# Kernel tuning notes

Measured on AMD Instinct MI355X. Metric: run time of the kernel, lower is better.

The kernel has to match this reference:

```python
import jax, jax.numpy as jnp
import numpy as np

B, T, V, D = 8, 256, 32, 256


def setup_inputs() -> dict:
    key = jax.random.key(0)
    k1, k2 = jax.random.split(key)
    # scale by 0.1 so exp(q.k) stays well within fp32 range (dot std ~ 0.1^2*sqrt(D))
    feature = jax.random.normal(k1, (B, T, V, D), dtype=jnp.float32) * 0.1
    feature_aug = jax.random.normal(k2, (B, T, V, D), dtype=jnp.float32) * 0.1
    return {"feature": feature, "feature_aug": feature_aug}


def reference(feature, feature_aug):
    # match torch permute(0,2,1,3): [B,T,V,D] -> [B,V,T,D]
    f = jnp.transpose(feature, (0, 2, 1, 3))      # [B,V,Tq,D]
    fa = jnp.transpose(feature_aug, (0, 2, 1, 3))  # [B,V,Tk,D]
    # all-pairs QK^T scores: [B_i, B_j, V, Tq, Tk]
    scores = jnp.einsum('ivqd,jvkd->ijvqk', f, fa)
    E = jnp.exp(scores)
    # positive (j == i): ap = exp(scores[i,i]).sum over V, Tq -> [B, Tk]
    diag = jnp.einsum('iivqk->ivqk', E)           # [B,V,Tq,Tk]
    ap_exp = diag.sum(axis=(1, 2))                # [B, Tk]
    # negatives (j != i): sum over j,V,Tk minus the j==i part -> [B, Tq]
    total = E.sum(axis=(1, 2, 4))                 # [B, Tq]
    self_part = diag.sum(axis=(1, 3))             # [B, Tq]
    an_exp = total - self_part                    # [B, Tq]
    # per-anchor loss vector [T]; original sums over anchors then takes .mean()
    loss_vec = -jnp.log(ap_exp / an_exp)          # [B, T]
    return loss_vec.sum(axis=0).mean()
```

## Files before the change

### kernel.cpp

```cpp
#include <hip/hip_runtime.h>
#include <hip/hip_bf16.h>


typedef __attribute__((ext_vector_type(4))) float f32x4;
typedef __attribute__((ext_vector_type(4))) int   i32x4;
typedef __attribute__((ext_vector_type(8))) int   i32x8;
typedef __attribute__((ext_vector_type(8))) __bf16 bf16x8;

#if __has_builtin(__builtin_amdgcn_exp2f)
#define EXP2(x) __builtin_amdgcn_exp2f(x)
#else
#define EXP2(x) exp2f(x)
#endif

__device__ __forceinline__ unsigned short f2bf(float f) {
    unsigned u = __builtin_bit_cast(unsigned, f);
    u += 0x7FFFu + ((u >> 16) & 1u);
    return (unsigned short)(u >> 16);
}

template <bool HI>
__device__ __forceinline__ unsigned cvt2fp8(float a, float b, unsigned old) {
    return __builtin_amdgcn_cvt_pk_fp8_f32(a, b, old, HI);
}
__device__ __forceinline__ unsigned pack4fp8(float x, float y, float z, float w) {
    return cvt2fp8<true>(z, w, cvt2fp8<false>(x, y, 0u));
}

__device__ __forceinline__ void async16(const void* g, void* l) {
    __builtin_amdgcn_global_load_lds(
        (const __attribute__((address_space(1))) unsigned int*)g,
        (__attribute__((address_space(3))) unsigned int*)l,
        16, 0, 0);
}

__device__ __forceinline__ i32x8 cat8(i32x4 lo, i32x4 hi) {
    i32x8 r;
    r[0] = lo[0]; r[1] = lo[1]; r[2] = lo[2]; r[3] = lo[3];
    r[4] = hi[0]; r[5] = hi[1]; r[6] = hi[2]; r[7] = hi[3];
    return r;
}

template <int CTRL>
__device__ __forceinline__ float dpp_add(float x) {
    int y = __builtin_amdgcn_update_dpp(0, __builtin_bit_cast(int, x),
                                        CTRL, 0xf, 0xf, true);
    return x + __builtin_bit_cast(float, y);
}
__device__ __forceinline__ float rowsum16(float x) {
    x = dpp_add<0x111>(x);
    x = dpp_add<0x112>(x);
    x = dpp_add<0x114>(x);
    x = dpp_add<0x118>(x);
    return x;
}

__global__ __launch_bounds__(256) void infonce_repack_fp8(
    const float* __restrict__ feat, const float* __restrict__ feat_aug,
    unsigned char* __restrict__ pA, unsigned char* __restrict__ pB,
    float* __restrict__ counters)
{
    const int row = blockIdx.x;
    const int tid = threadIdx.x;
    if (blockIdx.x == 0 && blockIdx.y == 0) {
        #pragma unroll
        for (int k = 0; k < 24; ++k) counters[k * 256 + tid] = 0.f;
    }
    const bool isA = (blockIdx.y == 0);
    const float sc = isA ? 1.4426950408889634f : 1.0f;
    const float* src = (isA ? feat : feat_aug) + (size_t)row * 8192;
    unsigned char* dst = (isA ? pA : pB) + (size_t)row * 8192;
    #pragma unroll
    for (int it = 0; it < 2; ++it) {
        const int base = it * 4096 + tid * 16;
        const float4 f0 = *(const float4*)(src + base);
        const float4 f1 = *(const float4*)(src + base + 4);
        const float4 f2 = *(const float4*)(src + base + 8);
        const float4 f3 = *(const float4*)(src + base + 12);
        uint4 p;
        p.x = pack4fp8(f0.x*sc, f0.y*sc, f0.z*sc, f0.w*sc);
        p.y = pack4fp8(f1.x*sc, f1.y*sc, f1.z*sc, f1.w*sc);
        p.z = pack4fp8(f2.x*sc, f2.y*sc, f2.z*sc, f2.w*sc);
        p.w = pack4fp8(f3.x*sc, f3.y*sc, f3.z*sc, f3.w*sc);
        *(uint4*)(dst + base) = p;
    }
}

__global__ __launch_bounds__(256, 2) void infonce_main_mx(
    const unsigned char* __restrict__ pA, const unsigned char* __restrict__ pB,
    float* __restrict__ total, float* __restrict__ selfp, float* __restrict__ ap)
{
    __shared__ __align__(16) unsigned char As[128 * 256];
    __shared__ __align__(16) unsigned char Bs[128 * 256];
    float (*ls_row2)[128] = (float (*)[128])(void*)As;
    float (*ls_col2)[128] = (float (*)[128])(void*)(As + 1024);

    const int tid  = threadIdx.x;
    const int lane = tid & 63;
    const int w    = tid >> 6;
    const int wm   = w >> 1;
    const int wn   = w & 1;
    const int lrow = lane & 15;
    const int quad = lane >> 4;

    const int tileM = blockIdx.x & 15;
    const int tileN = blockIdx.x >> 4;
    const int v     = blockIdx.y;
    const bool diag = (tileM >> 1) == (tileN >> 1);

    const size_t vOff = (size_t)v * 256;
    const size_t rowM = (size_t)(tileM * 128 + w * 32 + quad) * 8192 + vOff;
    const size_t rowN = (size_t)(tileN * 128 + w * 32 + quad) * 8192 + vOff;
    #pragma unroll
    for (int i = 0; i < 8; ++i) {
        const int lg = (lrow ^ ((i * 4 + quad) & 15)) << 4;
        async16(pA + rowM + (size_t)i * 4 * 8192 + lg, &As[(w * 32 + i * 4) * 256]);
        async16(pB + rowN + (size_t)i * 4 * 8192 + lg, &Bs[(w * 32 + i * 4) * 256]);
    }

    f32x4 acc[4][4];
    #pragma unroll
    for (int i = 0; i < 4; ++i)
        #pragma unroll
        for (int j = 0; j < 4; ++j)
            acc[i][j] = (f32x4){0.f, 0.f, 0.f, 0.f};

    __syncthreads();

    #pragma unroll
    for (int h = 0; h < 2; ++h) {
        const int g0 = ((h * 8 + quad * 2) ^ lrow) * 16;
        const int g1 = g0 ^ 16;
        i32x8 af[4], bf[4];
        #pragma unroll
        for (int t = 0; t < 4; ++t) {
            const int rA = (wm * 64 + t * 16 + lrow) * 256;
            const int rB = (wn * 64 + t * 16 + lrow) * 256;
            af[t] = cat8(*(const i32x4*)&As[rA + g0], *(const i32x4*)&As[rA + g1]);
            bf[t] = cat8(*(const i32x4*)&Bs[rB + g0], *(const i32x4*)&Bs[rB + g1]);
        }
        #pragma unroll
        for (int ti = 0; ti < 4; ++ti)
            #pragma unroll
            for (int tj = 0; tj < 4; ++tj)
                acc[ti][tj] = __builtin_amdgcn_mfma_scale_f32_16x16x128_f8f6f4(
                    af[ti], bf[tj], acc[ti][tj],
                    0, 0,
                    0, 127,
                    0, 127);
    }

    __syncthreads();

    float colp[4] = {0.f, 0.f, 0.f, 0.f};
    #pragma unroll
    for (int ti = 0; ti < 4; ++ti) {
        #pragma unroll
        for (int r = 0; r < 4; ++r) {
            float e0 = EXP2(acc[ti][0][r]);
            float e1 = EXP2(acc[ti][1][r]);
            float e2 = EXP2(acc[ti][2][r]);
            float e3 = EXP2(acc[ti][3][r]);
            if (diag) { colp[0] += e0; colp[1] += e1; colp[2] += e2; colp[3] += e3; }
            float rp = rowsum16((e0 + e1) + (e2 + e3));
            if (lrow == 15)
                ls_row2[wn][wm * 64 + ti * 16 + quad * 4 + r] = rp;
        }
    }
    if (diag) {
        #pragma unroll
        for (int tj = 0; tj < 4; ++tj) {
            float q = colp[tj];
            q += __shfl_xor(q, 16);
            q += __shfl_xor(q, 32);
            if (lane < 16)
                ls_col2[wm][wn * 64 + tj * 16 + lane] = q;
        }
    }
    __syncthreads();
    if (tid < 128) {
        const float rs = ls_row2[0][tid] + ls_row2[1][tid];
        const int rowg = tileM * 128 + tid;
        atomicAdd(&total[rowg], rs);
        if (diag) atomicAdd(&selfp[rowg], rs);
    } else if (diag) {
        const int t2 = tid - 128;
        atomicAdd(&ap[tileN * 128 + t2], ls_col2[0][t2] + ls_col2[1][t2]);
    }
}

__global__ __launch_bounds__(256) void infonce_main_slow(
    const float* __restrict__ feat, const float* __restrict__ feat_aug,
    float* __restrict__ total, float* __restrict__ selfp, float* __restrict__ ap)
{
    __shared__ __align__(16) unsigned short As[128][72];
    __shared__ __align__(16) unsigned short Bs[128][72];
    __shared__ float ls_row[128];
    __shared__ float ls_col[128];

    const int tid  = threadIdx.x;
    const int lane = tid & 63;
    const int w    = tid >> 6;
    const int wm   = w >> 1;
    const int wn   = w & 1;
    const int lrow = lane & 15;
    const int quad = lane >> 4;

    const int tileM = blockIdx.x & 15;
    const int tileN = blockIdx.x >> 4;
    const int v     = blockIdx.y;
    const bool diag = (tileM >> 1) == (tileN >> 1);

    if (tid < 128) ls_row[tid] = 0.0f;
    else           ls_col[tid - 128] = 0.0f;

    const float* aBase = feat     + (size_t)v * 256;
    const float* bBase = feat_aug + (size_t)v * 256;

    f32x4 acc[4][4];
    #pragma unroll
    for (int i = 0; i < 4; ++i)
        #pragma unroll
        for (int j = 0; j < 4; ++j)
            acc[i][j] = (f32x4){0.f, 0.f, 0.f, 0.f};

    const int srow = tid >> 4;
    const int scol = (tid & 15) * 4;

    for (int s = 0; s < 4; ++s) {
        const int k0 = s * 64;
        if (s) __syncthreads();
        #pragma unroll
        for (int it = 0; it < 8; ++it) {
            const int row = it * 16 + srow;
            const float4 a4 = *(const float4*)(aBase + (size_t)(tileM * 128 + row) * 8192 + k0 + scol);
            const float4 b4 = *(const float4*)(bBase + (size_t)(tileN * 128 + row) * 8192 + k0 + scol);
            uint2 wa, wb;
            wa.x = (unsigned)f2bf(a4.x) | ((unsigned)f2bf(a4.y) << 16);
            wa.y = (unsigned)f2bf(a4.z) | ((unsigned)f2bf(a4.w) << 16);
            wb.x = (unsigned)f2bf(b4.x) | ((unsigned)f2bf(b4.y) << 16);
            wb.y = (unsigned)f2bf(b4.z) | ((unsigned)f2bf(b4.w) << 16);
            *(uint2*)&As[row][scol] = wa;
            *(uint2*)&Bs[row][scol] = wb;
        }
        __syncthreads();
        #pragma unroll
        for (int kk = 0; kk < 64; kk += 32) {
            bf16x8 af[4], bfr[4];
            #pragma unroll
            for (int t = 0; t < 4; ++t) {
                af[t]  = *(const bf16x8*)&As[wm * 64 + t * 16 + lrow][kk + quad * 8];
                bfr[t] = *(const bf16x8*)&Bs[wn * 64 + t * 16 + lrow][kk + quad * 8];
            }
            #pragma unroll
            for (int ti = 0; ti < 4; ++ti)
                #pragma unroll
                for (int tj = 0; tj < 4; ++tj)
                    acc[ti][tj] = __builtin_amdgcn_mfma_f32_16x16x32_bf16(
                        af[ti], bfr[tj], acc[ti][tj], 0, 0, 0);
        }
    }

    float colp[4] = {0.f, 0.f, 0.f, 0.f};
    #pragma unroll
    for (int ti = 0; ti < 4; ++ti) {
        #pragma unroll
        for (int r = 0; r < 4; ++r) {
            float e0 = __expf(acc[ti][0][r]);
            float e1 = __expf(acc[ti][1][r]);
            float e2 = __expf(acc[ti][2][r]);
            float e3 = __expf(acc[ti][3][r]);
            colp[0] += e0; colp[1] += e1; colp[2] += e2; colp[3] += e3;
            float rp = (e0 + e1) + (e2 + e3);
            rp += __shfl_xor(rp, 1);
            rp += __shfl_xor(rp, 2);
            rp += __shfl_xor(rp, 4);
            rp += __shfl_xor(rp, 8);
            if (lrow == 0)
                atomicAdd(&ls_row[wm * 64 + ti * 16 + quad * 4 + r], rp);
        }
    }
    if (diag) {
        #pragma unroll
        for (int tj = 0; tj < 4; ++tj) {
            float q = colp[tj];
            q += __shfl_xor(q, 16);
            q += __shfl_xor(q, 32);
            if (lane < 16)
                atomicAdd(&ls_col[wn * 64 + tj * 16 + lane], q);
        }
    }
    __syncthreads();
    if (tid < 128) {
        const float rs = ls_row[tid];
        const int rowg = tileM * 128 + tid;
        atomicAdd(&total[rowg], rs);
        if (diag) atomicAdd(&selfp[rowg], rs);
    } else if (diag) {
        const int t2 = tid - 128;
        atomicAdd(&ap[tileN * 128 + t2], ls_col[t2]);
    }
}

__global__ __launch_bounds__(256) void infonce_finalize(
    const float* __restrict__ total, const float* __restrict__ selfp,
    const float* __restrict__ ap, float* __restrict__ out)
{
    __shared__ float red[4];
    const int tid = threadIdx.x;
    float s = 0.f;
    for (int e = tid; e < 2048; e += 256) {
        const float an = total[e] - selfp[e];
        s += logf(an / ap[e]);
    }
    #pragma unroll
    for (int m = 32; m >= 1; m >>= 1) s += __shfl_xor(s, m);
    if ((tid & 63) == 0) red[tid >> 6] = s;
    __syncthreads();
    if (tid == 0) out[0] = (red[0] + red[1] + red[2] + red[3]) * (1.0f / 256.0f);
}

extern "C" void kernel_launch(void* const* d_in, const int* in_sizes, int n_in,
                              void* d_out, int out_size, void* d_ws, size_t ws_size,
                              hipStream_t stream) {
    const float* feat     = (const float*)d_in[0];
    const float* feat_aug = (const float*)d_in[1];
    float* total = (float*)d_ws;
    float* selfp = total + 2048;
    float* ap    = selfp + 2048;

    const size_t packBytes = (size_t)2048 * 8192;
    const size_t need = 32768 + 2 * packBytes;
    if (ws_size >= need) {
        unsigned char* pA = (unsigned char*)d_ws + 32768;
        unsigned char* pB = pA + packBytes;
        infonce_repack_fp8<<<dim3(2048, 2), 256, 0, stream>>>(feat, feat_aug, pA, pB, total);
        infonce_main_mx<<<dim3(256, 32), 256, 0, stream>>>(pA, pB, total, selfp, ap);
    } else {
        (void)hipMemsetAsync(d_ws, 0, 3 * 2048 * sizeof(float), stream);
        infonce_main_slow<<<dim3(256, 32), 256, 0, stream>>>(feat, feat_aug, total, selfp, ap);
    }
    infonce_finalize<<<1, 256, 0, stream>>>(total, selfp, ap, (float*)d_out);
}
```

Baseline: 200.1 us.

## Keep A tile resident and stream B tiles with double-buffered async loads

The main fp8 MFMA kernel now launches one block per 128-row A tile and per V slice (16x32 blocks instead of 256x32). Each block keeps its A fragments in registers and loops over all 32 B sub-tiles of 64 rows, double-buffering them in shared memory with async loads. Row sums accumulate in registers across the loop, which removes repeated A loads and most per-tile global atomics. The cost is only 512 blocks on a large GPU, which may underfill the CUs, plus a serial loop with a barrier every iteration.

Result: faster. 193.4 us (-3.3%).

```diff
diff --git a/kernel.cpp b/kernel.cpp
--- a/kernel.cpp
+++ b/kernel.cpp
@@ -86,14 +86,14 @@
     }
 }
 
-__global__ __launch_bounds__(256, 2) void infonce_main_mx(
+__global__ __launch_bounds__(256, 2) void infonce_main_nl(
     const unsigned char* __restrict__ pA, const unsigned char* __restrict__ pB,
     float* __restrict__ total, float* __restrict__ selfp, float* __restrict__ ap)
 {
     __shared__ __align__(16) unsigned char As[128 * 256];
-    __shared__ __align__(16) unsigned char Bs[128 * 256];
-    float (*ls_row2)[128] = (float (*)[128])(void*)As;
-    float (*ls_col2)[128] = (float (*)[128])(void*)(As + 1024);
+    __shared__ __align__(16) unsigned char Bs[2][64 * 256];
+    float (*ls_row2)[128]  = (float (*)[128])(void*)As;
+    float (*ls_self2)[128] = (float (*)[128])(void*)(As + 1024);
 
     const int tid  = threadIdx.x;
     const int lane = tid & 63;
@@ -103,89 +103,123 @@
     const int lrow = lane & 15;
     const int quad = lane >> 4;
 
-    const int tileM = blockIdx.x & 15;
-    const int tileN = blockIdx.x >> 4;
+    const int tileM = blockIdx.x;
     const int v     = blockIdx.y;
-    const bool diag = (tileM >> 1) == (tileN >> 1);
+    const int nD0   = (tileM >> 1) * 4;
 
     const size_t vOff = (size_t)v * 256;
-    const size_t rowM = (size_t)(tileM * 128 + w * 32 + quad) * 8192 + vOff;
-    const size_t rowN = (size_t)(tileN * 128 + w * 32 + quad) * 8192 + vOff;
-    #pragma unroll
-    for (int i = 0; i < 8; ++i) {
+
+    {
+        const size_t rowM = (size_t)(tileM * 128 + w * 32 + quad) * 8192 + vOff;
+        #pragma unroll
+        for (int i = 0; i < 8; ++i) {
+            const int lg = (lrow ^ ((i * 4 + quad) & 15)) << 4;
+            async16(pA + rowM + (size_t)i * 4 * 8192 + lg, &As[(w * 32 + i * 4) * 256]);
+        }
+    }
+    const size_t rowNbase = (size_t)(w * 16 + quad) * 8192 + vOff;
+    #pragma unroll
+    for (int i = 0; i < 4; ++i) {
         const int lg = (lrow ^ ((i * 4 + quad) & 15)) << 4;
-        async16(pA + rowM + (size_t)i * 4 * 8192 + lg, &As[(w * 32 + i * 4) * 256]);
-        async16(pB + rowN + (size_t)i * 4 * 8192 + lg, &Bs[(w * 32 + i * 4) * 256]);
-    }
-
-    f32x4 acc[4][4];
-    #pragma unroll
-    for (int i = 0; i < 4; ++i)
-        #pragma unroll
-        for (int j = 0; j < 4; ++j)
-            acc[i][j] = (f32x4){0.f, 0.f, 0.f, 0.f};
-
+        async16(pB + rowNbase + (size_t)i * 4 * 8192 + lg,
+                &Bs[0][(w * 16 + i * 4) * 256]);
+    }
     __syncthreads();
 
-    #pragma unroll
-    for (int h = 0; h < 2; ++h) {
-        const int g0 = ((h * 8 + quad * 2) ^ lrow) * 16;
-        const int g1 = g0 ^ 16;
-        i32x8 af[4], bf[4];
+    i32x8 af[2][4];
+    #pragma unroll
+    for (int h = 0; h < 2; ++h)
         #pragma unroll
         for (int t = 0; t < 4; ++t) {
             const int rA = (wm * 64 + t * 16 + lrow) * 256;
-            const int rB = (wn * 64 + t * 16 + lrow) * 256;
-            af[t] = cat8(*(const i32x4*)&As[rA + g0], *(const i32x4*)&As[rA + g1]);
-            bf[t] = cat8(*(const i32x4*)&Bs[rB + g0], *(const i32x4*)&Bs[rB + g1]);
-        }
-        #pragma unroll
-        for (int ti = 0; ti < 4; ++ti)
-            #pragma unroll
-            for (int tj = 0; tj < 4; ++tj)
-                acc[ti][tj] = __builtin_amdgcn_mfma_scale_f32_16x16x128_f8f6f4(
-                    af[ti], bf[tj], acc[ti][tj],
-                    0, 0,
-                    0, 127,
-                    0, 127);
-    }
-
-    __syncthreads();
-
-    float colp[4] = {0.f, 0.f, 0.f, 0.f};
-    #pragma unroll
-    for (int ti = 0; ti < 4; ++ti) {
+            const int g0 = ((h * 8 + quad * 2) ^ lrow) * 16;
+            af[h][t] = cat8(*(const i32x4*)&As[rA + g0],
+                            *(const i32x4*)&As[rA + (g0 ^ 16)]);
+        }
+
+    float rowp[4][4];
+    float selfr[4][4];
+    #pragma unroll
+    for (int t = 0; t < 4; ++t)
+        #pragma unroll
+        for (int r = 0; r < 4; ++r) { rowp[t][r] = 0.f; selfr[t][r] = 0.f; }
+
+    for (int n = 0; n < 32; ++n) {
+        const int b = n & 1;
+        if (n < 31) {
+            const unsigned char* src = pB + rowNbase + (size_t)(n + 1) * 64 * 8192;
+            #pragma unroll
+            for (int i = 0; i < 4; ++i) {
+                const int lg = (lrow ^ ((i * 4 + quad) & 15)) << 4;
+                async16(src + (size_t)i * 4 * 8192 + lg,
+                        &Bs[b ^ 1][(w * 16 + i * 4) * 256]);
+            }
+        }
+        f32x4 acc[4][2];
+        #pragma unroll
+        for (int t = 0; t < 4; ++t)
+            #pragma unroll
+            for (int tj = 0; tj < 2; ++tj)
+                acc[t][tj] = (f32x4){0.f, 0.f, 0.f, 0.f};
+        #pragma unroll
+        for (int h = 0; h < 2; ++h) {
+            i32x8 bf[2];
+            #pragma unroll
+            for (int tj = 0; tj < 2; ++tj) {
+                const int rB = (wn * 32 + tj * 16 + lrow) * 256;
+                const int g0 = ((h * 8 + quad * 2) ^ lrow) * 16;
+                bf[tj] = cat8(*(const i32x4*)&Bs[b][rB + g0],
+                              *(const i32x4*)&Bs[b][rB + (g0 ^ 16)]);
+            }
+            #pragma unroll
+            for (int ti = 0; ti < 4; ++ti)
+                #pragma unroll
+                for (int tj = 0; tj < 2; ++tj)
+                    acc[ti][tj] = __builtin_amdgcn_mfma_scale_f32_16x16x128_f8f6f4(
+                        af[h][ti], bf[tj], acc[ti][tj],
+                        0, 0, 0, 127, 0, 127);
+        }
+        const bool diagIter = (n >= nD0) && (n < nD0 + 4);
+        float colp0 = 0.f, colp1 = 0.f;
+        #pragma unroll
+        for (int t = 0; t < 4; ++t)
+            #pragma unroll
+            for (int r = 0; r < 4; ++r) {
+                float e0 = EXP2(acc[t][0][r]);
+                float e1 = EXP2(acc[t][1][r]);
+                rowp[t][r] += e0 + e1;
+                if (diagIter) { selfr[t][r] += e0 + e1; colp0 += e0; colp1 += e1; }
+            }
+        if (diagIter) {
+            float q0 = colp0, q1 = colp1;
+            q0 += __shfl_xor(q0, 16); q0 += __shfl_xor(q0, 32);
+            q1 += __shfl_xor(q1, 16); q1 += __shfl_xor(q1, 32);
+            if (lane < 16) {
+                atomicAdd(&ap[n * 64 + wn * 32 + lane], q0);
+                atomicAdd(&ap[n * 64 + wn * 32 + 16 + lane], q1);
+            }
+        }
+        __syncthreads();
+    }
+
+    #pragma unroll
+    for (int t = 0; t < 4; ++t)
         #pragma unroll
         for (int r = 0; r < 4; ++r) {
-            float e0 = EXP2(acc[ti][0][r]);
-            float e1 = EXP2(acc[ti][1][r]);
-            float e2 = EXP2(acc[ti][2][r]);
-            float e3 = EXP2(acc[ti][3][r]);
-            if (diag) { colp[0] += e0; colp[1] += e1; colp[2] += e2; colp[3] += e3; }
-            float rp = rowsum16((e0 + e1) + (e2 + e3));
-            if (lrow == 15)
-                ls_row2[wn][wm * 64 + ti * 16 + quad * 4 + r] = rp;
-        }
-    }
-    if (diag) {
-        #pragma unroll
-        for (int tj = 0; tj < 4; ++tj) {
-            float q = colp[tj];
-            q += __shfl_xor(q, 16);
-            q += __shfl_xor(q, 32);
-            if (lane < 16)
-                ls_col2[wm][wn * 64 + tj * 16 + lane] = q;
-        }
-    }
+            float rs = rowsum16(rowp[t][r]);
+            float ss = rowsum16(selfr[t][r]);
+            if (lrow == 15) {
+                const int idx = wm * 64 + t * 16 + quad * 4 + r;
+                ls_row2[wn][idx]  = rs;
+                ls_self2[wn][idx] = ss;
+            }
+        }
     __syncthreads();
     if (tid < 128) {
-        const float rs = ls_row2[0][tid] + ls_row2[1][tid];
-        const int rowg = tileM * 128 + tid;
-        atomicAdd(&total[rowg], rs);
-        if (diag) atomicAdd(&selfp[rowg], rs);
-    } else if (diag) {
+        atomicAdd(&total[tileM * 128 + tid], ls_row2[0][tid] + ls_row2[1][tid]);
+    } else {
         const int t2 = tid - 128;
-        atomicAdd(&ap[tileN * 128 + t2], ls_col2[0][t2] + ls_col2[1][t2]);
+        atomicAdd(&selfp[tileM * 128 + t2], ls_self2[0][t2] + ls_self2[1][t2]);
     }
 }
 
@@ -335,7 +369,7 @@
         unsigned char* pA = (unsigned char*)d_ws + 32768;
         unsigned char* pB = pA + packBytes;
         infonce_repack_fp8<<<dim3(2048, 2), 256, 0, stream>>>(feat, feat_aug, pA, pB, total);
-        infonce_main_mx<<<dim3(256, 32), 256, 0, stream>>>(pA, pB, total, selfp, ap);
+        infonce_main_nl<<<dim3(16, 32), 256, 0, stream>>>(pA, pB, total, selfp, ap);
     } else {
         (void)hipMemsetAsync(d_ws, 0, 3 * 2048 * sizeof(float), stream);
         infonce_main_slow<<<dim3(256, 32), 256, 0, stream>>>(feat, feat_aug, total, selfp, ap);
```
